# Kernel tuning notes

Hardware: AMD Instinct MI355X
Metric: run time of the kernel (lower is better)

Reference implementation:

```python
import jax, jax.numpy as jnp
import numpy as np

NUM_HEADS = 8
OUT_FEATS = 128
D_HEAD = OUT_FEATS // NUM_HEADS
N_NODES = 50000
N_EDGES = 600000
IN_FEATS = 128


def setup_inputs() -> dict:
    key = jax.random.key(0)
    ks = jax.random.split(key, 10)
    h = jax.random.normal(ks[0], (N_NODES, IN_FEATS), dtype=jnp.float32)
    src = jax.random.randint(ks[1], (N_EDGES,), 0, N_NODES)
    dst = jax.random.randint(ks[2], (N_EDGES,), 0, N_NODES)
    s = 1.0 / np.sqrt(IN_FEATS)
    W_Q = jax.random.normal(ks[3], (IN_FEATS, OUT_FEATS), dtype=jnp.float32) * s
    W_K = jax.random.normal(ks[4], (IN_FEATS, OUT_FEATS), dtype=jnp.float32) * s
    W_V = jax.random.normal(ks[5], (IN_FEATS, OUT_FEATS), dtype=jnp.float32) * s
    b_Q = jnp.zeros((OUT_FEATS,), dtype=jnp.float32)
    b_K = jnp.zeros((OUT_FEATS,), dtype=jnp.float32)
    b_V = jnp.zeros((OUT_FEATS,), dtype=jnp.float32)
    return {"h": h, "W_Q": W_Q, "b_Q": b_Q, "W_K": W_K, "b_K": b_K,
            "W_V": W_V, "b_V": b_V, "src": src, "dst": dst}


def _graph_conv(h, W, b, src, dst, norm_src, norm_dst):
    # DGL GraphConv, norm='both': D_dst^{-1/2} * A * D_src^{-1/2} * (h W) + b
    x = (h * norm_src[:, None]) @ W                              # [N, F]
    agg = jax.ops.segment_sum(x[src], dst, num_segments=h.shape[0])
    return agg * norm_dst[:, None] + b


def reference(h, W_Q, b_Q, W_K, b_K, W_V, b_V, src, dst):
    N = h.shape[0]
    ones = jnp.ones(src.shape[0], dtype=h.dtype)
    deg_out = jax.ops.segment_sum(ones, src, num_segments=N)   # out-degree (src side)
    deg_in = jax.ops.segment_sum(ones, dst, num_segments=N)    # in-degree (dst side)
    norm_src = jax.lax.rsqrt(jnp.clip(deg_out, 1.0))
    norm_dst = jax.lax.rsqrt(jnp.clip(deg_in, 1.0))

    Q = jax.nn.relu(_graph_conv(h, W_Q, b_Q, src, dst, norm_src, norm_dst))
    K = jax.nn.relu(_graph_conv(h, W_K, b_K, src, dst, norm_src, norm_dst))
    V = jax.nn.relu(_graph_conv(h, W_V, b_V, src, dst, norm_src, norm_dst))

    Qh = Q.reshape(N, NUM_HEADS, D_HEAD)
    Kh = K.reshape(N, NUM_HEADS, D_HEAD)
    Vh = V.reshape(N, NUM_HEADS, D_HEAD)

    # edge-wise scores: K at src dotted with Q at dst, per head
    score = jnp.sum(Kh[src] * Qh[dst], axis=-1, keepdims=True)   # [E, H, 1]
    score = jnp.exp(jnp.clip(score / np.sqrt(D_HEAD), -10.0, 10.0))

    wV = jax.ops.segment_sum(Vh[src] * score, dst, num_segments=N)  # [N, H, Dh]
    z = jax.ops.segment_sum(score, dst, num_segments=N)             # [N, H, 1]
    return wV / (z + 1e-6)
```

## Files before the change

### kernel.cpp

```cpp
#include <hip/hip_runtime.h>

#define INF  128
#define OUTF 128
#define NH   8
#define DHD  16
#define CAP  48
#define TPAD 132

typedef __attribute__((ext_vector_type(8))) short bf16x8;
typedef __attribute__((ext_vector_type(4))) float f32x4;

__device__ __forceinline__ float bf16_to_f32(unsigned short u) {
    union { unsigned int i; float f; } v;
    v.i = ((unsigned int)u) << 16;
    return v.f;
}
__device__ __forceinline__ unsigned short f32_to_bf16(float f) {
    union { float f; unsigned int i; } v;
    v.f = f;
    unsigned int x = v.i;
    return (unsigned short)((x + 0x7fffu + ((x >> 16) & 1u)) >> 16);
}

__global__ void k_front(const int* __restrict__ src, const int* __restrict__ dst,
                        int* __restrict__ deg_out, int* __restrict__ cursor,
                        int* __restrict__ edge_src, int E, int SB, int HB,
                        const float* __restrict__ h, unsigned short* __restrict__ h_b, int N,
                        const float* __restrict__ Wq, const float* __restrict__ Wk,
                        const float* __restrict__ Wv, unsigned short* __restrict__ frag) {
    if (blockIdx.x < (unsigned)SB) {
        int t = blockIdx.x * 256 + threadIdx.x;
        if (t < E) {
            int s = src[t];
            int d = dst[t];
            atomicAdd(&deg_out[s], 1);
            int p = atomicAdd(&cursor[d], 1);
            if (p < CAP) edge_src[d * CAP + p] = s;
        }
    } else if (blockIdx.x < (unsigned)(SB + HB)) {
        int t = (blockIdx.x - SB) * 256 + threadIdx.x;
        if (t < N * (INF / 8)) {
            const float4* p = reinterpret_cast<const float4*>(h + (size_t)t * 8);
            float4 v0 = p[0], v1 = p[1];
            uint4 o;
            o.x = (unsigned int)f32_to_bf16(v0.x) | ((unsigned int)f32_to_bf16(v0.y) << 16);
            o.y = (unsigned int)f32_to_bf16(v0.z) | ((unsigned int)f32_to_bf16(v0.w) << 16);
            o.z = (unsigned int)f32_to_bf16(v1.x) | ((unsigned int)f32_to_bf16(v1.y) << 16);
            o.w = (unsigned int)f32_to_bf16(v1.z) | ((unsigned int)f32_to_bf16(v1.w) << 16);
            *reinterpret_cast<uint4*>(h_b + (size_t)t * 8) = o;
        }
    } else {
        int t = (blockIdx.x - SB - HB) * 256 + threadIdx.x;
        if (t >= 3 * 8 * 4 * 2 * 64) return;
        int lane  = t & 63;
        int plane = (t >> 6) & 1;
        int ks    = (t >> 7) & 3;
        int nt    = (t >> 9) & 7;
        int mat   = t >> 12;
        const float* W = (mat == 0) ? Wq : ((mat == 1) ? Wk : Wv);
        int ln = lane & 15, quad = lane >> 4;
        int n = nt * 16 + ln;
        unsigned short vals[8];
        #pragma unroll
        for (int j = 0; j < 8; ++j) {
            int k = ks * 32 + quad * 8 + j;
            float a = W[k * OUTF + n];
            unsigned short hb = f32_to_bf16(a);
            vals[j] = plane ? f32_to_bf16(a - bf16_to_f32(hb)) : hb;
        }
        unsigned int* dp = reinterpret_cast<unsigned int*>(frag + (size_t)t * 8);
        #pragma unroll
        for (int j = 0; j < 4; ++j)
            dp[j] = (unsigned int)vals[2 * j] | ((unsigned int)vals[2 * j + 1] << 16);
    }
}

__global__ __launch_bounds__(256) void k_aggemm(const unsigned short* __restrict__ h_b,
                                                const int* __restrict__ deg_out,
                                                const int* __restrict__ cursor,
                                                const int* __restrict__ edge_src,
                                                const unsigned short* __restrict__ frag,
                                                const float* __restrict__ bq,
                                                const float* __restrict__ bk,
                                                const float* __restrict__ bv,
                                                float* __restrict__ qbuf,
                                                unsigned short* __restrict__ kvbuf,
                                                int N) {
    __shared__ float tile[4][16][TPAD];
    int wave = threadIdx.x >> 6;
    int lane = threadIdx.x & 63;
    int half = lane >> 5, li = lane & 31;
    int c4   = li * 4;
    int mrow = blockIdx.x * 64 + wave * 16;

    for (int r = 0; r < 16; ++r) {
        int node = mrow + r;
        float a0 = 0.f, a1 = 0.f, a2 = 0.f, a3 = 0.f;
        if (node < N) {
            int deg = cursor[node]; if (deg > CAP) deg = CAP;
            const int* rowp = edge_src + node * CAP;
            auto proc = [&](int e) {
                int s = rowp[e];
                int dg = deg_out[s]; if (dg < 1) dg = 1;
                float ns = rsqrtf((float)dg);
                uint2 p = *reinterpret_cast<const uint2*>(h_b + (size_t)s * INF + c4);
                a0 += ns * bf16_to_f32((unsigned short)(p.x & 0xffffu));
                a1 += ns * bf16_to_f32((unsigned short)(p.x >> 16));
                a2 += ns * bf16_to_f32((unsigned short)(p.y & 0xffffu));
                a3 += ns * bf16_to_f32((unsigned short)(p.y >> 16));
            };
            int e = half;
            for (; e + 4 <= deg; e += 4) { proc(e); proc(e + 2); }
            for (; e < deg; e += 2) proc(e);
        }
        a0 += __shfl_xor(a0, 32);
        a1 += __shfl_xor(a1, 32);
        a2 += __shfl_xor(a2, 32);
        a3 += __shfl_xor(a3, 32);
        if (half == 0)
            *reinterpret_cast<float4*>(&tile[wave][r][c4]) = make_float4(a0, a1, a2, a3);
    }

    int ln   = lane & 15;
    int quad = lane >> 4;
    bf16x8 ah[4], al[4];
    {
        const float* trow = &tile[wave][ln][0];
        #pragma unroll
        for (int ks = 0; ks < 4; ++ks) {
            const float4* p = reinterpret_cast<const float4*>(trow + ks * 32 + quad * 8);
            float4 v0 = p[0], v1 = p[1];
            float vv[8] = {v0.x, v0.y, v0.z, v0.w, v1.x, v1.y, v1.z, v1.w};
            #pragma unroll
            for (int j = 0; j < 8; ++j) {
                unsigned short hb = f32_to_bf16(vv[j]);
                ah[ks][j] = (short)hb;
                al[ks][j] = (short)f32_to_bf16(vv[j] - bf16_to_f32(hb));
            }
        }
    }

    float nrm[4];
    #pragma unroll
    for (int r = 0; r < 4; ++r) {
        int m = mrow + quad * 4 + r;
        if (m < N) {
            int dg = cursor[m]; if (dg < 1) dg = 1;
            nrm[r] = rsqrtf((float)dg);
        } else nrm[r] = 0.f;
    }

    #pragma unroll
    for (int mat = 0; mat < 3; ++mat) {
        const float* bb = (mat == 0) ? bq : ((mat == 1) ? bk : bv);
        #pragma unroll 2
        for (int nt = 0; nt < 8; ++nt) {
            f32x4 acc = {0.f, 0.f, 0.f, 0.f};
            #pragma unroll
            for (int ks = 0; ks < 4; ++ks) {
                size_t base = ((size_t)(((mat * 8 + nt) * 4 + ks) * 2) * 64 + lane) * 8;
                bf16x8 bh = *reinterpret_cast<const bf16x8*>(frag + base);
                bf16x8 bl = *reinterpret_cast<const bf16x8*>(frag + base + 64 * 8);
                acc = __builtin_amdgcn_mfma_f32_16x16x32_bf16(ah[ks], bh, acc, 0, 0, 0);
                acc = __builtin_amdgcn_mfma_f32_16x16x32_bf16(al[ks], bh, acc, 0, 0, 0);
                acc = __builtin_amdgcn_mfma_f32_16x16x32_bf16(ah[ks], bl, acc, 0, 0, 0);
            }
            int col = nt * 16 + ln;
            float bias = bb[col];
            #pragma unroll
            for (int r = 0; r < 4; ++r) {
                int m = mrow + quad * 4 + r;
                if (m < N) {
                    float v = acc[r] * nrm[r] + bias;
                    v = (v > 0.f) ? v : 0.f;
                    if (mat == 0) {
                        qbuf[(size_t)m * OUTF + col] = v;
                    } else {
                        int idx = ((col >> 2) << 3) + (col & 3) + ((mat == 2) ? 4 : 0);
                        kvbuf[(size_t)m * 2 * OUTF + idx] = f32_to_bf16(v);
                    }
                }
            }
        }
    }
}

__global__ __launch_bounds__(256) void k_attn(const float* __restrict__ qbuf,
                                              const unsigned short* __restrict__ kvbuf,
                                              const int* __restrict__ cursor,
                                              const int* __restrict__ edge_src,
                                              float* __restrict__ out, int N) {
    int wid  = (blockIdx.x * 256 + threadIdx.x) >> 6;
    int lane = threadIdx.x & 63;
    if (wid >= N) return;
    int half = lane >> 5, li = lane & 31;
    int c4 = li * 4;
    float4 q = *reinterpret_cast<const float4*>(qbuf + (size_t)wid * OUTF + c4);
    float a0 = 0.f, a1 = 0.f, a2 = 0.f, a3 = 0.f, z = 0.f;
    int deg = cursor[wid]; if (deg > CAP) deg = CAP;
    const int* row = edge_src + wid * CAP;
    auto proc = [&](int e) {
        int s = row[e];
        uint4 kp = *reinterpret_cast<const uint4*>(kvbuf + (size_t)s * 2 * OUTF + li * 8);
        float p = q.x * bf16_to_f32((unsigned short)(kp.x & 0xffffu))
                + q.y * bf16_to_f32((unsigned short)(kp.x >> 16))
                + q.z * bf16_to_f32((unsigned short)(kp.y & 0xffffu))
                + q.w * bf16_to_f32((unsigned short)(kp.y >> 16));
        p += __shfl_xor(p, 1);
        p += __shfl_xor(p, 2);
        float w = __expf(fminf(fmaxf(0.25f * p, -10.f), 10.f));
        z  += w;
        a0 += w * bf16_to_f32((unsigned short)(kp.z & 0xffffu));
        a1 += w * bf16_to_f32((unsigned short)(kp.z >> 16));
        a2 += w * bf16_to_f32((unsigned short)(kp.w & 0xffffu));
        a3 += w * bf16_to_f32((unsigned short)(kp.w >> 16));
    };
    int e = half;
    for (; e + 4 <= deg; e += 4) { proc(e); proc(e + 2); }
    for (; e < deg; e += 2) proc(e);
    a0 += __shfl_xor(a0, 32);
    a1 += __shfl_xor(a1, 32);
    a2 += __shfl_xor(a2, 32);
    a3 += __shfl_xor(a3, 32);
    z  += __shfl_xor(z, 32);
    if (half == 0) {
        float inv = 1.0f / (z + 1e-6f);
        *reinterpret_cast<float4*>(out + (size_t)wid * OUTF + c4) =
            make_float4(a0 * inv, a1 * inv, a2 * inv, a3 * inv);
    }
}

extern "C" void kernel_launch(void* const* d_in, const int* in_sizes, int n_in,
                              void* d_out, int out_size, void* d_ws, size_t ws_size,
                              hipStream_t stream) {
    const float* h  = (const float*)d_in[0];
    const float* Wq = (const float*)d_in[1];
    const float* bq = (const float*)d_in[2];
    const float* Wk = (const float*)d_in[3];
    const float* bk = (const float*)d_in[4];
    const float* Wv = (const float*)d_in[5];
    const float* bv = (const float*)d_in[6];
    const int* src = (const int*)d_in[7];
    const int* dst = (const int*)d_in[8];

    const int N = in_sizes[0] / INF;
    const int E = in_sizes[7];

    char* ws = (char*)d_ws;
    size_t off = 0;
    auto carve = [&](size_t bytes) -> void* {
        void* p = ws + off;
        off = (off + bytes + 255) & ~(size_t)255;
        return p;
    };
    int*   zeroed    = (int*)  carve((size_t)2 * N * sizeof(int));
    int*   deg_out   = zeroed;
    int*   cursor    = zeroed + N;
    int*   edge_src  = (int*)  carve((size_t)N * CAP * sizeof(int));
    unsigned short* h_b  = (unsigned short*)carve((size_t)N * INF * sizeof(unsigned short));
    float* qbuf      = (float*)carve((size_t)N * OUTF * sizeof(float));
    unsigned short* kvbuf = (unsigned short*)carve((size_t)N * 2 * OUTF * sizeof(unsigned short));
    unsigned short* wfrag = (unsigned short*)carve((size_t)3 * 8 * 4 * 2 * 64 * 8 * sizeof(unsigned short));
    (void)ws_size;

    float* out = (float*)d_out;

    hipMemsetAsync(zeroed, 0, (size_t)2 * N * sizeof(int), stream);

    int SB = (E + 255) / 256;
    int HB = (N * (INF / 8) + 255) / 256;
    int WB = (3 * 8 * 4 * 2 * 64 + 255) / 256;
    k_front<<<SB + HB + WB, 256, 0, stream>>>(src, dst, deg_out, cursor, edge_src,
                                              E, SB, HB, h, h_b, N, Wq, Wk, Wv, wfrag);

    int gFuse = (N + 63) / 64;
    k_aggemm<<<gFuse, 256, 0, stream>>>(h_b, deg_out, cursor, edge_src, wfrag,
                                        bq, bk, bv, qbuf, kvbuf, N);

    int gAttn = (N + 3) / 4;
    k_attn<<<gAttn, 256, 0, stream>>>(qbuf, kvbuf, cursor, edge_src, out, N);
}
```

Baseline: 282.4 us.

## Gather neighbor features directly into MFMA fragment layout, drop LDS tile

The neighbor aggregation now runs with each lane owning one node row and the 32 feature columns it needs for the MFMA A-fragment, accumulated in registers. This removes the shared-memory staging tile, the cross-half shuffle reduction and the LDS round trip before the matrix multiply. In exchange each lane walks its node's edge list serially, so lanes in a wave diverge when degrees differ and per-lane loads are strided rather than coalesced across the row. Register pressure also rises with 32 float accumulators per lane.

```diff
diff --git a/kernel.cpp b/kernel.cpp
--- a/kernel.cpp
+++ b/kernel.cpp
@@ -5,7 +5,6 @@
 #define NH   8
 #define DHD  16
 #define CAP  48
-#define TPAD 132
 
 typedef __attribute__((ext_vector_type(8))) short bf16x8;
 typedef __attribute__((ext_vector_type(4))) float f32x4;
@@ -86,59 +85,54 @@
                                                 float* __restrict__ qbuf,
                                                 unsigned short* __restrict__ kvbuf,
                                                 int N) {
-    __shared__ float tile[4][16][TPAD];
     int wave = threadIdx.x >> 6;
     int lane = threadIdx.x & 63;
-    int half = lane >> 5, li = lane & 31;
-    int c4   = li * 4;
-    int mrow = blockIdx.x * 64 + wave * 16;
-
-    for (int r = 0; r < 16; ++r) {
-        int node = mrow + r;
-        float a0 = 0.f, a1 = 0.f, a2 = 0.f, a3 = 0.f;
-        if (node < N) {
-            int deg = cursor[node]; if (deg > CAP) deg = CAP;
-            const int* rowp = edge_src + node * CAP;
-            auto proc = [&](int e) {
-                int s = rowp[e];
-                int dg = deg_out[s]; if (dg < 1) dg = 1;
-                float ns = rsqrtf((float)dg);
-                uint2 p = *reinterpret_cast<const uint2*>(h_b + (size_t)s * INF + c4);
-                a0 += ns * bf16_to_f32((unsigned short)(p.x & 0xffffu));
-                a1 += ns * bf16_to_f32((unsigned short)(p.x >> 16));
-                a2 += ns * bf16_to_f32((unsigned short)(p.y & 0xffffu));
-                a3 += ns * bf16_to_f32((unsigned short)(p.y >> 16));
-            };
-            int e = half;
-            for (; e + 4 <= deg; e += 4) { proc(e); proc(e + 2); }
-            for (; e < deg; e += 2) proc(e);
-        }
-        a0 += __shfl_xor(a0, 32);
-        a1 += __shfl_xor(a1, 32);
-        a2 += __shfl_xor(a2, 32);
-        a3 += __shfl_xor(a3, 32);
-        if (half == 0)
-            *reinterpret_cast<float4*>(&tile[wave][r][c4]) = make_float4(a0, a1, a2, a3);
-    }
-
     int ln   = lane & 15;
     int quad = lane >> 4;
+    int mrow = blockIdx.x * 64 + wave * 16;
+    int node = mrow + ln;
+
+    float acc_a[4][8];
+    #pragma unroll
+    for (int ks = 0; ks < 4; ++ks)
+        #pragma unroll
+        for (int j = 0; j < 8; ++j) acc_a[ks][j] = 0.f;
+
+    int deg = 0;
+    const int* rowp = edge_src + (size_t)node * CAP;
+    if (node < N) { deg = cursor[node]; if (deg > CAP) deg = CAP; }
+
+    auto proc = [&](int e) {
+        int s = rowp[e];
+        int dg = deg_out[s]; if (dg < 1) dg = 1;
+        float ns = rsqrtf((float)dg);
+        const unsigned short* hrow = h_b + (size_t)s * INF + quad * 8;
+        #pragma unroll
+        for (int ks = 0; ks < 4; ++ks) {
+            uint4 v = *reinterpret_cast<const uint4*>(hrow + ks * 32);
+            acc_a[ks][0] += ns * bf16_to_f32((unsigned short)(v.x & 0xffffu));
+            acc_a[ks][1] += ns * bf16_to_f32((unsigned short)(v.x >> 16));
+            acc_a[ks][2] += ns * bf16_to_f32((unsigned short)(v.y & 0xffffu));
+            acc_a[ks][3] += ns * bf16_to_f32((unsigned short)(v.y >> 16));
+            acc_a[ks][4] += ns * bf16_to_f32((unsigned short)(v.z & 0xffffu));
+            acc_a[ks][5] += ns * bf16_to_f32((unsigned short)(v.z >> 16));
+            acc_a[ks][6] += ns * bf16_to_f32((unsigned short)(v.w & 0xffffu));
+            acc_a[ks][7] += ns * bf16_to_f32((unsigned short)(v.w >> 16));
+        }
+    };
+    int e = 0;
+    for (; e + 2 <= deg; e += 2) { proc(e); proc(e + 1); }
+    if (e < deg) proc(e);
+
     bf16x8 ah[4], al[4];
-    {
-        const float* trow = &tile[wave][ln][0];
-        #pragma unroll
-        for (int ks = 0; ks < 4; ++ks) {
-            const float4* p = reinterpret_cast<const float4*>(trow + ks * 32 + quad * 8);
-            float4 v0 = p[0], v1 = p[1];
-            float vv[8] = {v0.x, v0.y, v0.z, v0.w, v1.x, v1.y, v1.z, v1.w};
-            #pragma unroll
-            for (int j = 0; j < 8; ++j) {
-                unsigned short hb = f32_to_bf16(vv[j]);
-                ah[ks][j] = (short)hb;
-                al[ks][j] = (short)f32_to_bf16(vv[j] - bf16_to_f32(hb));
-            }
-        }
-    }
+    #pragma unroll
+    for (int ks = 0; ks < 4; ++ks)
+        #pragma unroll
+        for (int j = 0; j < 8; ++j) {
+            unsigned short hb = f32_to_bf16(acc_a[ks][j]);
+            ah[ks][j] = (short)hb;
+            al[ks][j] = (short)f32_to_bf16(acc_a[ks][j] - bf16_to_f32(hb));
+        }
 
     float nrm[4];
     #pragma unroll
```

Measured after the change: 257.8 us. 8.7% less time.
